# Optimization experiments

Measured on AMD Instinct MI355X. Metric: run time of the kernel, lower is better.

Reference implementation:

```python
import jax, jax.numpy as jnp
import numpy as np

N, E, G, H = 50000, 800000, 2048, 128
DIS = 3  # dis_emb is None -> raw frac_diff (3 dims)
EIN = 2 * H + 6 + DIS  # 265


def _lin_init(key, fan_in, fan_out):
    lim = 1.0 / np.sqrt(fan_in)
    return jax.random.uniform(key, (fan_in, fan_out), jnp.float32, -lim, lim)


def setup_inputs() -> dict:
    key = jax.random.key(0)
    ks = jax.random.split(key, 12)
    node_features = jax.random.normal(ks[0], (N, H), jnp.float32)
    frac_coords = jax.random.uniform(ks[1], (N, 3), jnp.float32)
    lattices = jax.random.normal(ks[2], (G, 6), jnp.float32)
    frac_diff = jax.random.normal(ks[3], (E, 3), jnp.float32)
    edge_index = jax.random.randint(ks[4], (2, E), 0, N, jnp.int64 if jax.config.jax_enable_x64 else jnp.int32)
    edge2graph = jax.random.randint(ks[5], (E,), 0, G, edge_index.dtype)
    return dict(
        node_features=node_features,
        frac_coords=frac_coords,
        lattices=lattices,
        frac_diff=frac_diff,
        edge_index=edge_index,
        edge2graph=edge2graph,
        e_w1=_lin_init(ks[6], EIN, H), e_b1=jnp.zeros((H,), jnp.float32),
        e_w2=_lin_init(ks[7], H, H), e_b2=jnp.zeros((H,), jnp.float32),
        n_w1=_lin_init(ks[8], 2 * H, H), n_b1=jnp.zeros((H,), jnp.float32),
        n_w2=_lin_init(ks[9], H, H), n_b2=jnp.zeros((H,), jnp.float32),
    )


def reference(node_features, frac_coords, lattices, frac_diff, edge_index, edge2graph,
              e_w1, e_b1, e_w2, e_b2, n_w1, n_b1, n_w2, n_b2):
    n_nodes = node_features.shape[0]
    silu = jax.nn.silu
    # edge model: gather endpoints, concat with per-graph lattice + frac_diff
    hi = node_features[edge_index[0]]            # [E, H]
    hj = node_features[edge_index[1]]            # [E, H]
    lat = lattices[edge2graph]                   # [E, 6]
    edges_input = jnp.concatenate([hi, hj, lat, frac_diff], axis=1)  # [E, 265]
    e = silu(edges_input @ e_w1 + e_b1)
    edge_features = silu(e @ e_w2 + e_b2)        # [E, H]
    # scatter-mean aggregate onto source nodes
    seg = edge_index[0]
    agg_sum = jax.ops.segment_sum(edge_features, seg, num_segments=n_nodes)
    cnt = jax.ops.segment_sum(jnp.ones((edge_features.shape[0],), edge_features.dtype), seg, num_segments=n_nodes)
    agg = agg_sum / jnp.maximum(cnt, 1.0)[:, None]
    # node model + residual
    h = jnp.concatenate([node_features, agg], axis=1)  # [N, 2H]
    h = silu(h @ n_w1 + n_b1)
    node_output = silu(h @ n_w2 + n_b2)
    return node_features + node_output
```

## Files before the change

### kernel.cpp

```cpp
#include <hip/hip_runtime.h>

#define N_NODES 50000
#define N_EDGES 800000
#define HDIM 128
#define N_GRAPH 2048

typedef __bf16 bf16x8 __attribute__((ext_vector_type(8)));
typedef float f32x4 __attribute__((ext_vector_type(4)));
typedef float f32x16 __attribute__((ext_vector_type(16)));

static __device__ __forceinline__ unsigned short f2bf(float f) {
    unsigned int u = __float_as_uint(f);
    u += 0x7fffu + ((u >> 16) & 1u);
    return (unsigned short)(u >> 16);
}
static __device__ __forceinline__ float bflo(unsigned int u) { return __uint_as_float(u << 16); }
static __device__ __forceinline__ float bfhi(unsigned int u) { return __uint_as_float(u & 0xFFFF0000u); }

static __device__ __forceinline__ unsigned int cvt_pk_bf16(float lo, float hi) {
    unsigned int r;
    asm("v_cvt_pk_bf16_f32 %0, %1, %2" : "=v"(r) : "v"(lo), "v"(hi));
    return r;
}

static __device__ __forceinline__ float silu_f(float x) {
    float e = __builtin_amdgcn_exp2f(x * -1.44269504f);
    return x * __builtin_amdgcn_rcpf(1.0f + e);
}

#define PREP_BLOCKS 1408
#define HIST_BLOCKS 3125
#define ZERO_BLOCKS 6250
__global__ void prep_hist_kernel(const float* __restrict__ ew1, const float* __restrict__ ew2,
                                 const float* __restrict__ nw1, const float* __restrict__ nw2,
                                 const float* __restrict__ eb1, const float* __restrict__ lattices,
                                 const int* __restrict__ eidx,
                                 unsigned short* __restrict__ W1aT, unsigned short* __restrict__ W1bT,
                                 unsigned short* __restrict__ W2t, unsigned short* __restrict__ N1t,
                                 unsigned short* __restrict__ N2t, unsigned short* __restrict__ Lb,
                                 int* __restrict__ buf, float* __restrict__ agg) {
    const int bid = blockIdx.x;
    if (bid >= PREP_BLOCKS + HIST_BLOCKS) {
        const int idx = (bid - PREP_BLOCKS - HIST_BLOCKS) * 256 + threadIdx.x;
        ((float4*)agg)[idx] = make_float4(0.f, 0.f, 0.f, 0.f);
        return;
    }
    if (bid >= PREP_BLOCKS) {
        int e = (bid - PREP_BLOCKS) * 256 + threadIdx.x;
        if (e < N_EDGES) atomicAdd(&buf[eidx[e]], 1);
        return;
    }
    int i = bid * 256 + threadIdx.x;
    if (i < 16384) {
        int n = i >> 7, k = i & 127;
        W1aT[i] = f2bf(ew1[k * 128 + n]);
    } else if (i < 32768) {
        int j = i - 16384; int n = j >> 7, k = j & 127;
        W1bT[j] = f2bf(ew1[(128 + k) * 128 + n]);
    } else if (i < 49152) {
        int j = i - 32768; int n = j >> 7, k = j & 127;
        W2t[j] = f2bf(ew2[k * 128 + n]);
    } else if (i < 81920) {
        int j = i - 49152; int n = j >> 8, k = j & 255;
        N1t[j] = f2bf(nw1[k * 128 + n]);
    } else if (i < 98304) {
        int j = i - 81920; int n = j >> 7, k = j & 127;
        N2t[j] = f2bf(nw2[k * 128 + n]);
    } else if (i < 98304 + 262144) {
        int j = i - 98304; int g = j >> 7, c = j & 127;
        float s = eb1[c];
#pragma unroll
        for (int t = 0; t < 6; ++t) s += lattices[g * 6 + t] * ew1[(256 + t) * 128 + c];
        Lb[j] = f2bf(s);
    }
}

__global__ __launch_bounds__(1024) void scan_kernel(int* __restrict__ buf) {
    constexpr int CH = 12288;
    __shared__ int lds[CH];
    __shared__ int part[1024];
    __shared__ int carry_s;
    const int t = threadIdx.x;
    if (t == 0) carry_s = 0;
    __syncthreads();
#pragma unroll 1
    for (int base = 0; base < N_NODES; base += CH) {
#pragma unroll
        for (int k = 0; k < CH / 1024; ++k) {
            int f = k * 1024 + t;
            lds[f] = (base + f < N_NODES) ? buf[base + f] : 0;
        }
        __syncthreads();
        int loc[12];
        int s = 0;
#pragma unroll
        for (int i = 0; i < 12; ++i) { loc[i] = lds[t * 12 + i]; s += loc[i]; }
        part[t] = s;
        __syncthreads();
        for (int off = 1; off < 1024; off <<= 1) {
            int tmp = (t >= off) ? part[t - off] : 0;
            __syncthreads();
            part[t] += tmp;
            __syncthreads();
        }
        const int total = part[1023];
        int run = carry_s + part[t] - s;
#pragma unroll
        for (int i = 0; i < 12; ++i) { int tmp = loc[i]; lds[t * 12 + i] = run; run += tmp; }
        __syncthreads();
#pragma unroll
        for (int k = 0; k < CH / 1024; ++k) {
            int f = k * 1024 + t;
            if (base + f < N_NODES) buf[base + f] = lds[f];
        }
        __syncthreads();
        if (t == 0) carry_s += total;
        __syncthreads();
    }
}

#define PERM_BLOCKS2 3125
#define PQ_BLOCKS ((N_NODES + 63) / 64)
__global__ __launch_bounds__(256, 4) void perm_pq_kernel(
    const int* __restrict__ eidx, const int* __restrict__ e2g,
    const float* __restrict__ frac_diff, int* __restrict__ buf,
    unsigned short* __restrict__ perm_lo, unsigned char* __restrict__ perm_hi,
    uint4* __restrict__ rec, const int packed,
    const float* __restrict__ nf, const unsigned short* __restrict__ W1aT,
    const unsigned short* __restrict__ W1bT,
    unsigned short* __restrict__ P, unsigned short* __restrict__ Qm) {
    constexpr int SA = 136;
    __shared__ unsigned short sm[64 * SA];
    const int bid = blockIdx.x;
    const int tid = threadIdx.x;

    if (bid < PERM_BLOCKS2) {
        int e = bid * 256 + tid;
        if (e < N_EDGES) {
            int s = eidx[e];
            int pos = atomicAdd(&buf[s], 1);
            if (packed) {
                int d = eidx[N_EDGES + e];
                int g = e2g[e];
                unsigned int w0 = (unsigned int)s | ((unsigned int)d << 16);
                unsigned int w1 = (unsigned int)g | ((unsigned int)f2bf(frac_diff[3 * e]) << 16);
                unsigned int w2 = (unsigned int)f2bf(frac_diff[3 * e + 1]) |
                                  ((unsigned int)f2bf(frac_diff[3 * e + 2]) << 16);
                rec[pos] = make_uint4(w0, w1, w2, 0u);
            } else {
                perm_lo[pos] = (unsigned short)(e & 0xFFFF);
                perm_hi[pos] = (unsigned char)(e >> 16);
            }
        }
        return;
    }

    const int n0 = (bid - PERM_BLOCKS2) * 64;
    const int mrow = tid >> 2, q = tid & 3;
    {
        const int node = n0 + mrow;
        unsigned short* row = sm + mrow * SA + q * 32;
        if (node < N_NODES) {
            const float4* a4 = (const float4*)(nf + (size_t)node * HDIM) + q * 8;
#pragma unroll
            for (int j = 0; j < 8; ++j) {
                float4 v = a4[j];
                *(ushort4*)(row + 4 * j) = make_ushort4(f2bf(v.x), f2bf(v.y), f2bf(v.z), f2bf(v.w));
            }
        } else {
#pragma unroll
            for (int j = 0; j < 8; ++j) *(ushort4*)(row + 4 * j) = make_ushort4(0, 0, 0, 0);
        }
    }
    __syncthreads();

    const int wave = tid >> 6, lane = tid & 63;
    const int lr = lane & 15, kq = lane >> 4;
    f32x4 acca[8] = {}, accb[8] = {};
    const int arow = (wave * 16 + lr) * SA;
#pragma unroll
    for (int ks = 0; ks < 128; ks += 32) {
        bf16x8 a = *(const bf16x8*)(sm + arow + ks + kq * 8);
#pragma unroll
        for (int nt = 0; nt < 8; ++nt) {
            bf16x8 ba = *(const bf16x8*)(W1aT + (nt * 16 + lr) * 128 + ks + kq * 8);
            acca[nt] = __builtin_amdgcn_mfma_f32_16x16x32_bf16(a, ba, acca[nt], 0, 0, 0);
            bf16x8 bb = *(const bf16x8*)(W1bT + (nt * 16 + lr) * 128 + ks + kq * 8);
            accb[nt] = __builtin_amdgcn_mfma_f32_16x16x32_bf16(a, bb, accb[nt], 0, 0, 0);
        }
    }
    __syncthreads();

    const int node = n0 + mrow;
#pragma unroll
    for (int nt = 0; nt < 8; ++nt) {
        const int col = nt * 16 + lr;
#pragma unroll
        for (int r = 0; r < 4; ++r)
            sm[(wave * 16 + kq * 4 + r) * SA + col] = f2bf(acca[nt][r]);
    }
    __syncthreads();
    if (node < N_NODES) {
        uint4* dst = (uint4*)(P + (size_t)node * HDIM + q * 32);
        const uint4* srcp = (const uint4*)(sm + mrow * SA + q * 32);
#pragma unroll
        for (int j = 0; j < 4; ++j) dst[j] = srcp[j];
    }
    __syncthreads();
#pragma unroll
    for (int nt = 0; nt < 8; ++nt) {
        const int col = nt * 16 + lr;
#pragma unroll
        for (int r = 0; r < 4; ++r)
            sm[(wave * 16 + kq * 4 + r) * SA + col] = f2bf(accb[nt][r]);
    }
    __syncthreads();
    if (node < N_NODES) {
        uint4* dst = (uint4*)(Qm + (size_t)node * HDIM + q * 32);
        const uint4* srcp = (const uint4*)(sm + mrow * SA + q * 32);
#pragma unroll
        for (int j = 0; j < 4; ++j) dst[j] = srcp[j];
    }
}

#define EDGE_NWG (N_EDGES / 128)
template <bool PACKED>
__global__ __launch_bounds__(256, 3) void edge_kernel(
    const unsigned short* __restrict__ P, const unsigned short* __restrict__ Qm,
    const unsigned short* __restrict__ Lb, const float* __restrict__ frac_diff,
    const int* __restrict__ eidx, const int* __restrict__ e2g,
    const unsigned short* __restrict__ perm_lo, const unsigned char* __restrict__ perm_hi,
    const uint4* __restrict__ rec,
    const float* __restrict__ e_w1, const unsigned short* __restrict__ W2t,
    const float* __restrict__ b2, float* __restrict__ agg) {
    const int tid = threadIdx.x;
    const int wv = tid >> 6, lane = tid & 63;
    const int row = lane & 31, hi = lane >> 5;
    const int base = blockIdx.x * 128 + wv * 32;

    int src, dst, g;
    float fd0, fd1, fd2;
    if (PACKED) {
        const uint4 rv = rec[base + row];
        src = rv.x & 0xFFFF;
        dst = rv.x >> 16;
        g = rv.y & 0xFFFF;
        fd0 = bfhi(rv.y);
        fd1 = bflo(rv.z);
        fd2 = bfhi(rv.z);
    } else {
        const int i = base + row;
        const int e = (int)perm_lo[i] | ((int)perm_hi[i] << 16);
        src = eidx[e];
        dst = eidx[N_EDGES + e];
        g = e2g[e];
        fd0 = frac_diff[3 * e];
        fd1 = frac_diff[3 * e + 1];
        fd2 = frac_diff[3 * e + 2];
    }

    const size_t prow = (size_t)src * HDIM;
    const size_t qrow = (size_t)dst * HDIM;
    const size_t lrow = (size_t)g * HDIM;
    uint4 pu[8], qu[8], lu[8];
#pragma unroll
    for (int kk = 0; kk < 8; ++kk) {
        const int c0 = kk * 16 + hi * 8;
        pu[kk] = *(const uint4*)(P + prow + c0);
        qu[kk] = *(const uint4*)(Qm + qrow + c0);
        lu[kk] = *(const uint4*)(Lb + lrow + c0);
    }

    int sc[16], snq[4];
#pragma unroll
    for (int r = 0; r < 16; ++r)
        sc[r] = __shfl(src, (r & 3) + 8 * (r >> 2) + 4 * hi);
#pragma unroll
    for (int j = 0; j < 4; ++j)
        snq[j] = __shfl(src, (4 * (2 * j + hi) + 4) & 31);

    const float* wrbase = e_w1 + 262 * HDIM;
    bf16x8 afrag[8];
#pragma unroll
    for (int kk = 0; kk < 8; ++kk) {
        const int c0 = kk * 16 + hi * 8;
        float w0[8], w1[8], w2[8];
        *(float4*)(w0) = *(const float4*)(wrbase + c0);
        *(float4*)(w0 + 4) = *(const float4*)(wrbase + c0 + 4);
        *(float4*)(w1) = *(const float4*)(wrbase + 128 + c0);
        *(float4*)(w1 + 4) = *(const float4*)(wrbase + 128 + c0 + 4);
        *(float4*)(w2) = *(const float4*)(wrbase + 256 + c0);
        *(float4*)(w2 + 4) = *(const float4*)(wrbase + 256 + c0 + 4);
        const unsigned int* pw = (const unsigned int*)&pu[kk];
        const unsigned int* qw = (const unsigned int*)&qu[kk];
        const unsigned int* lw = (const unsigned int*)&lu[kk];
        unsigned int ow[4];
#pragma unroll
        for (int w = 0; w < 4; ++w) {
            float x0 = bflo(pw[w]) + bflo(qw[w]) + bflo(lw[w])
                     + fd0 * w0[2 * w] + fd1 * w1[2 * w] + fd2 * w2[2 * w];
            float x1 = bfhi(pw[w]) + bfhi(qw[w]) + bfhi(lw[w])
                     + fd0 * w0[2 * w + 1] + fd1 * w1[2 * w + 1] + fd2 * w2[2 * w + 1];
            ow[w] = cvt_pk_bf16(silu_f(x0), silu_f(x1));
        }
        afrag[kk] = *(bf16x8*)ow;
    }

    f32x16 acc[4] = {};
#pragma unroll
    for (int kk = 0; kk < 8; ++kk) {
#pragma unroll
        for (int t4 = 0; t4 < 4; ++t4) {
            bf16x8 bb = *(const bf16x8*)(W2t + (t4 * 32 + row) * 128 + kk * 16 + hi * 8);
            acc[t4] = __builtin_amdgcn_mfma_f32_32x32x16_bf16(afrag[kk], bb, acc[t4], 0, 0, 0);
        }
    }

#pragma unroll
    for (int t4 = 0; t4 < 4; ++t4) {
        const int col = t4 * 32 + row;
        const float bias = b2[col];
        float p[16], tq[4], to[4];
#pragma unroll
        for (int rq = 0; rq < 4; ++rq) {
            float s0 = silu_f(acc[t4][4 * rq + 0] + bias);
            float s1 = silu_f(acc[t4][4 * rq + 1] + bias);
            float s2 = silu_f(acc[t4][4 * rq + 2] + bias);
            float s3 = silu_f(acc[t4][4 * rq + 3] + bias);
            p[4 * rq + 0] = s0;
            p[4 * rq + 1] = s0 + s1;
            p[4 * rq + 2] = p[4 * rq + 1] + s2;
            p[4 * rq + 3] = p[4 * rq + 2] + s3;
            tq[rq] = p[4 * rq + 3];
            to[rq] = __shfl_xor(tq[rq], 32);
        }
        float cum = 0.f;
#pragma unroll
        for (int rq = 0; rq < 4; ++rq) {
            const float off = cum + (hi ? to[rq] : 0.f);
            cum += tq[rq] + to[rq];
#pragma unroll
            for (int i = 0; i < 4; ++i) {
                const int r = 4 * rq + i;
                const float val = p[r] + off;
                const int myrow = 4 * (2 * rq + hi) + i;
                const bool lastg = (myrow == 31);
                const int nxt = (i < 3) ? sc[r + 1] : snq[rq];
                const bool bnd = lastg || (sc[r] != nxt);
                if (bnd) {
                    atomicAdd(&agg[(size_t)sc[r] * HDIM + col], val);
                    if (!lastg) atomicAdd(&agg[(size_t)nxt * HDIM + col], -val);
                }
            }
        }
    }
}

__global__ __launch_bounds__(256, 4) void node_kernel(
    const float* __restrict__ nf, const float* __restrict__ agg,
    const int* __restrict__ buf,
    const unsigned short* __restrict__ N1t, const float* __restrict__ b1,
    const unsigned short* __restrict__ N2t, const float* __restrict__ b2,
    float* __restrict__ out) {
    constexpr int SA = 264;
    constexpr int S2 = 136;
    constexpr int SFo = 132;
    __shared__ unsigned short sm[64 * SA];
    float* smf = (float*)sm;

    const int tid = threadIdx.x;
    const int n0 = blockIdx.x * 64;
    const int mrow = tid >> 2, q = tid & 3;
    {
        const int node = n0 + mrow;
        unsigned short* row = sm + mrow * SA;
        const int cbq = q * 32;
        if (node < N_NODES) {
            const int c = buf[node] - (node ? buf[node - 1] : 0);
            const float inv = 1.0f / (float)max(c, 1);
            const float4* a4 = (const float4*)(nf + (size_t)node * HDIM) + q * 8;
            const float4* g4 = (const float4*)(agg + (size_t)node * HDIM) + q * 8;
#pragma unroll
            for (int j = 0; j < 8; ++j) {
                float4 v = a4[j];
                *(ushort4*)(row + cbq + 4 * j) =
                    make_ushort4(f2bf(v.x), f2bf(v.y), f2bf(v.z), f2bf(v.w));
                float4 g = g4[j];
                *(ushort4*)(row + HDIM + cbq + 4 * j) =
                    make_ushort4(f2bf(g.x * inv), f2bf(g.y * inv), f2bf(g.z * inv), f2bf(g.w * inv));
            }
        } else {
#pragma unroll
            for (int j = 0; j < 8; ++j) {
                *(ushort4*)(row + cbq + 4 * j) = make_ushort4(0, 0, 0, 0);
                *(ushort4*)(row + HDIM + cbq + 4 * j) = make_ushort4(0, 0, 0, 0);
            }
        }
    }
    __syncthreads();

    const int wave = tid >> 6, lane = tid & 63;
    const int lr = lane & 15, kq = lane >> 4;

    f32x4 acc[8] = {};
    const int arow = (wave * 16 + lr) * SA;
#pragma unroll
    for (int ks = 0; ks < 256; ks += 32) {
        bf16x8 a = *(const bf16x8*)(sm + arow + ks + kq * 8);
#pragma unroll
        for (int nt = 0; nt < 8; ++nt) {
            bf16x8 bb = *(const bf16x8*)(N1t + (nt * 16 + lr) * 256 + ks + kq * 8);
            acc[nt] = __builtin_amdgcn_mfma_f32_16x16x32_bf16(a, bb, acc[nt], 0, 0, 0);
        }
    }
    __syncthreads();

#pragma unroll
    for (int nt = 0; nt < 8; ++nt) {
        const int col = nt * 16 + lr;
        const float bias = b1[col];
#pragma unroll
        for (int r = 0; r < 4; ++r) {
            const int mm = wave * 16 + kq * 4 + r;
            sm[mm * S2 + col] = f2bf(silu_f(acc[nt][r] + bias));
        }
    }
    __syncthreads();

    f32x4 acc2[8] = {};
    const int arow2 = (wave * 16 + lr) * S2;
#pragma unroll
    for (int ks = 0; ks < 128; ks += 32) {
        bf16x8 a = *(const bf16x8*)(sm + arow2 + ks + kq * 8);
#pragma unroll
        for (int nt = 0; nt < 8; ++nt) {
            bf16x8 bb = *(const bf16x8*)(N2t + (nt * 16 + lr) * 128 + ks + kq * 8);
            acc2[nt] = __builtin_amdgcn_mfma_f32_16x16x32_bf16(a, bb, acc2[nt], 0, 0, 0);
        }
    }
    __syncthreads();

#pragma unroll
    for (int nt = 0; nt < 8; ++nt) {
        const int col = nt * 16 + lr;
        const float bias = b2[col];
#pragma unroll
        for (int r = 0; r < 4; ++r) {
            const int mm = wave * 16 + kq * 4 + r;
            smf[mm * SFo + col] = silu_f(acc2[nt][r] + bias);
        }
    }
    __syncthreads();
    {
        const int node = n0 + mrow;
        if (node < N_NODES) {
            const float4* nfr = (const float4*)(nf + (size_t)node * HDIM) + q * 8;
            float4* outr = (float4*)(out + (size_t)node * HDIM) + q * 8;
            const float* st = smf + mrow * SFo + q * 32;
#pragma unroll
            for (int j = 0; j < 8; ++j) {
                float4 v = nfr[j];
                float4 s4 = *(const float4*)(st + 4 * j);
                v.x += s4.x; v.y += s4.y; v.z += s4.z; v.w += s4.w;
                outr[j] = v;
            }
        }
    }
}

extern "C" void kernel_launch(void* const* d_in, const int* in_sizes, int n_in,
                              void* d_out, int out_size, void* d_ws, size_t ws_size,
                              hipStream_t stream) {
    const float* node_features = (const float*)d_in[0];
    const float* lattices = (const float*)d_in[2];
    const float* frac_diff = (const float*)d_in[3];
    const int* edge_index = (const int*)d_in[4];
    const int* edge2graph = (const int*)d_in[5];
    const float* e_w1 = (const float*)d_in[6];
    const float* e_b1 = (const float*)d_in[7];
    const float* e_w2 = (const float*)d_in[8];
    const float* e_b2 = (const float*)d_in[9];
    const float* n_w1 = (const float*)d_in[10];
    const float* n_b1 = (const float*)d_in[11];
    const float* n_w2 = (const float*)d_in[12];
    const float* n_b2 = (const float*)d_in[13];

    char* ws = (char*)d_ws;
    unsigned short* W1aT = (unsigned short*)(ws);
    unsigned short* W1bT = (unsigned short*)(ws + 32768);
    unsigned short* W2t  = (unsigned short*)(ws + 65536);
    unsigned short* N1t  = (unsigned short*)(ws + 98304);
    unsigned short* N2t  = (unsigned short*)(ws + 163840);
    unsigned short* Lb   = (unsigned short*)(ws + 196608);
    unsigned short* P    = (unsigned short*)(ws + 720896);
    unsigned short* Qm   = (unsigned short*)(ws + 13520896);
    int* buf             = (int*)(ws + 26320896);
    unsigned short* perm_lo = (unsigned short*)(ws + 26520896);
    unsigned char* perm_hi  = (unsigned char*)(ws + 28120896);
    uint4* rec           = (uint4*)(ws + 28920896);
    float* agg = (float*)d_out;

    const int packed = (ws_size >= 28920896 + (size_t)N_EDGES * 16) ? 1 : 0;

    hipMemsetAsync(buf, 0, (size_t)N_NODES * 4, stream);

    prep_hist_kernel<<<PREP_BLOCKS + HIST_BLOCKS + ZERO_BLOCKS, 256, 0, stream>>>(
        e_w1, e_w2, n_w1, n_w2, e_b1, lattices, edge_index,
        W1aT, W1bT, W2t, N1t, N2t, Lb, buf, agg);

    scan_kernel<<<1, 1024, 0, stream>>>(buf);

    perm_pq_kernel<<<PERM_BLOCKS2 + PQ_BLOCKS, 256, 0, stream>>>(
        edge_index, edge2graph, frac_diff, buf, perm_lo, perm_hi, rec, packed,
        node_features, W1aT, W1bT, P, Qm);

    if (packed) {
        edge_kernel<true><<<EDGE_NWG, 256, 0, stream>>>(
            P, Qm, Lb, frac_diff, edge_index, edge2graph, perm_lo, perm_hi, rec,
            e_w1, W2t, e_b2, agg);
    } else {
        edge_kernel<false><<<EDGE_NWG, 256, 0, stream>>>(
            P, Qm, Lb, frac_diff, edge_index, edge2graph, perm_lo, perm_hi, rec,
            e_w1, W2t, e_b2, agg);
    }

    node_kernel<<<(N_NODES + 63) / 64, 256, 0, stream>>>(
        node_features, agg, buf, N1t, n_b1, N2t, n_b2, (float*)d_out);
}
```

Baseline: 544.4 us.

## Process two 32-edge tiles per wave with prefetched gathers and LDS-staged frac weights

Each wave in the edge kernel now handles two 32-edge tiles and issues the gathers for both tiles up front, so the second tile's global loads overlap with the first tile's compute. The frac_diff rows of the first-layer weights are converted to bf16 once per block and read from LDS, replacing per-lane fp32 global loads. The price is more registers per wave (occupancy bound drops from 3 to 2), one block-wide barrier, and slightly lower precision on those weights.

Result: faster. 515.1 us (-5.4%).

```diff
diff --git a/kernel.cpp b/kernel.cpp
--- a/kernel.cpp
+++ b/kernel.cpp
@@ -223,90 +223,39 @@
     }
 }
 
-#define EDGE_NWG (N_EDGES / 128)
-template <bool PACKED>
-__global__ __launch_bounds__(256, 3) void edge_kernel(
-    const unsigned short* __restrict__ P, const unsigned short* __restrict__ Qm,
-    const unsigned short* __restrict__ Lb, const float* __restrict__ frac_diff,
-    const int* __restrict__ eidx, const int* __restrict__ e2g,
-    const unsigned short* __restrict__ perm_lo, const unsigned char* __restrict__ perm_hi,
-    const uint4* __restrict__ rec,
-    const float* __restrict__ e_w1, const unsigned short* __restrict__ W2t,
-    const float* __restrict__ b2, float* __restrict__ agg) {
-    const int tid = threadIdx.x;
-    const int wv = tid >> 6, lane = tid & 63;
-    const int row = lane & 31, hi = lane >> 5;
-    const int base = blockIdx.x * 128 + wv * 32;
-
-    int src, dst, g;
-    float fd0, fd1, fd2;
-    if (PACKED) {
-        const uint4 rv = rec[base + row];
-        src = rv.x & 0xFFFF;
-        dst = rv.x >> 16;
-        g = rv.y & 0xFFFF;
-        fd0 = bfhi(rv.y);
-        fd1 = bflo(rv.z);
-        fd2 = bfhi(rv.z);
-    } else {
-        const int i = base + row;
-        const int e = (int)perm_lo[i] | ((int)perm_hi[i] << 16);
-        src = eidx[e];
-        dst = eidx[N_EDGES + e];
-        g = e2g[e];
-        fd0 = frac_diff[3 * e];
-        fd1 = frac_diff[3 * e + 1];
-        fd2 = frac_diff[3 * e + 2];
-    }
-
-    const size_t prow = (size_t)src * HDIM;
-    const size_t qrow = (size_t)dst * HDIM;
-    const size_t lrow = (size_t)g * HDIM;
-    uint4 pu[8], qu[8], lu[8];
+
+static __device__ __forceinline__ void build_afrag(
+    const uint4* pu, const uint4* qu, const uint4* lu,
+    float f0, float f1, float f2,
+    const unsigned int* wlds, int hi, bf16x8* afrag) {
 #pragma unroll
     for (int kk = 0; kk < 8; ++kk) {
-        const int c0 = kk * 16 + hi * 8;
-        pu[kk] = *(const uint4*)(P + prow + c0);
-        qu[kk] = *(const uint4*)(Qm + qrow + c0);
-        lu[kk] = *(const uint4*)(Lb + lrow + c0);
-    }
-
-    int sc[16], snq[4];
-#pragma unroll
-    for (int r = 0; r < 16; ++r)
-        sc[r] = __shfl(src, (r & 3) + 8 * (r >> 2) + 4 * hi);
-#pragma unroll
-    for (int j = 0; j < 4; ++j)
-        snq[j] = __shfl(src, (4 * (2 * j + hi) + 4) & 31);
-
-    const float* wrbase = e_w1 + 262 * HDIM;
-    bf16x8 afrag[8];
-#pragma unroll
-    for (int kk = 0; kk < 8; ++kk) {
-        const int c0 = kk * 16 + hi * 8;
-        float w0[8], w1[8], w2[8];
-        *(float4*)(w0) = *(const float4*)(wrbase + c0);
-        *(float4*)(w0 + 4) = *(const float4*)(wrbase + c0 + 4);
-        *(float4*)(w1) = *(const float4*)(wrbase + 128 + c0);
-        *(float4*)(w1 + 4) = *(const float4*)(wrbase + 128 + c0 + 4);
-        *(float4*)(w2) = *(const float4*)(wrbase + 256 + c0);
-        *(float4*)(w2 + 4) = *(const float4*)(wrbase + 256 + c0 + 4);
+        const unsigned int* wl = wlds + (kk * 2 + hi) * 12;
+        const uint4 w0v = *(const uint4*)(wl);
+        const uint4 w1v = *(const uint4*)(wl + 4);
+        const uint4 w2v = *(const uint4*)(wl + 8);
         const unsigned int* pw = (const unsigned int*)&pu[kk];
         const unsigned int* qw = (const unsigned int*)&qu[kk];
         const unsigned int* lw = (const unsigned int*)&lu[kk];
+        const unsigned int* w0w = (const unsigned int*)&w0v;
+        const unsigned int* w1w = (const unsigned int*)&w1v;
+        const unsigned int* w2w = (const unsigned int*)&w2v;
         unsigned int ow[4];
 #pragma unroll
         for (int w = 0; w < 4; ++w) {
             float x0 = bflo(pw[w]) + bflo(qw[w]) + bflo(lw[w])
-                     + fd0 * w0[2 * w] + fd1 * w1[2 * w] + fd2 * w2[2 * w];
+                     + f0 * bflo(w0w[w]) + f1 * bflo(w1w[w]) + f2 * bflo(w2w[w]);
             float x1 = bfhi(pw[w]) + bfhi(qw[w]) + bfhi(lw[w])
-                     + fd0 * w0[2 * w + 1] + fd1 * w1[2 * w + 1] + fd2 * w2[2 * w + 1];
+                     + f0 * bfhi(w0w[w]) + f1 * bfhi(w1w[w]) + f2 * bfhi(w2w[w]);
             ow[w] = cvt_pk_bf16(silu_f(x0), silu_f(x1));
         }
         afrag[kk] = *(bf16x8*)ow;
     }
-
-    f32x16 acc[4] = {};
+}
+
+static __device__ __forceinline__ void do_mfma(
+    const bf16x8* afrag, const unsigned short* __restrict__ W2t,
+    int row, int hi, f32x16* acc) {
 #pragma unroll
     for (int kk = 0; kk < 8; ++kk) {
 #pragma unroll
@@ -315,7 +264,11 @@
             acc[t4] = __builtin_amdgcn_mfma_f32_32x32x16_bf16(afrag[kk], bb, acc[t4], 0, 0, 0);
         }
     }
-
+}
+
+static __device__ __forceinline__ void epilogue(
+    const f32x16* acc, const int* sc, const int* snq,
+    int row, int hi, const float* __restrict__ b2, float* __restrict__ agg) {
 #pragma unroll
     for (int t4 = 0; t4 < 4; ++t4) {
         const int col = t4 * 32 + row;
@@ -354,6 +307,112 @@
             }
         }
     }
+}
+
+#define EDGE_NWG (N_EDGES / 256)
+template <bool PACKED>
+static __device__ __forceinline__ void fetch_meta(
+    int i, const uint4* __restrict__ rec, const int* __restrict__ eidx,
+    const int* __restrict__ e2g, const float* __restrict__ frac_diff,
+    const unsigned short* __restrict__ perm_lo, const unsigned char* __restrict__ perm_hi,
+    int& src, int& dst, int& g, float& f0, float& f1, float& f2) {
+    if (PACKED) {
+        const uint4 rv = rec[i];
+        src = rv.x & 0xFFFF;
+        dst = rv.x >> 16;
+        g = rv.y & 0xFFFF;
+        f0 = bfhi(rv.y);
+        f1 = bflo(rv.z);
+        f2 = bfhi(rv.z);
+    } else {
+        const int e = (int)perm_lo[i] | ((int)perm_hi[i] << 16);
+        src = eidx[e];
+        dst = eidx[N_EDGES + e];
+        g = e2g[e];
+        f0 = frac_diff[3 * e];
+        f1 = frac_diff[3 * e + 1];
+        f2 = frac_diff[3 * e + 2];
+    }
+}
+
+template <bool PACKED>
+__global__ __launch_bounds__(256, 2) void edge_kernel(
+    const unsigned short* __restrict__ P, const unsigned short* __restrict__ Qm,
+    const unsigned short* __restrict__ Lb, const float* __restrict__ frac_diff,
+    const int* __restrict__ eidx, const int* __restrict__ e2g,
+    const unsigned short* __restrict__ perm_lo, const unsigned char* __restrict__ perm_hi,
+    const uint4* __restrict__ rec,
+    const float* __restrict__ e_w1, const unsigned short* __restrict__ W2t,
+    const float* __restrict__ b2, float* __restrict__ agg) {
+    __shared__ __align__(16) unsigned int wlds[192];
+    const int tid = threadIdx.x;
+    {
+        const float* wrbase = e_w1 + 262 * HDIM;
+        if (tid < 192) {
+            const int w = tid & 3, rw = (tid >> 2) % 3, hi = (tid / 12) & 1, kk = tid / 24;
+            const int c = kk * 16 + hi * 8 + 2 * w;
+            wlds[((kk * 2 + hi) * 3 + rw) * 4 + w] =
+                (unsigned int)f2bf(wrbase[rw * HDIM + c]) |
+                ((unsigned int)f2bf(wrbase[rw * HDIM + c + 1]) << 16);
+        }
+    }
+    __syncthreads();
+
+    const int wv = tid >> 6, lane = tid & 63;
+    const int row = lane & 31, hi = lane >> 5;
+    const int base = blockIdx.x * 256 + wv * 64;
+
+    int srcA, dstA, gA; float fA0, fA1, fA2;
+    fetch_meta<PACKED>(base + row, rec, eidx, e2g, frac_diff, perm_lo, perm_hi,
+                       srcA, dstA, gA, fA0, fA1, fA2);
+    int srcB, dstB, gB; float fB0, fB1, fB2;
+    fetch_meta<PACKED>(base + 32 + row, rec, eidx, e2g, frac_diff, perm_lo, perm_hi,
+                       srcB, dstB, gB, fB0, fB1, fB2);
+
+    uint4 puA[8], quA[8], luA[8];
+    {
+        const size_t pr = (size_t)srcA * HDIM, qr = (size_t)dstA * HDIM, lr = (size_t)gA * HDIM;
+#pragma unroll
+        for (int kk = 0; kk < 8; ++kk) {
+            const int c0 = kk * 16 + hi * 8;
+            puA[kk] = *(const uint4*)(P + pr + c0);
+            quA[kk] = *(const uint4*)(Qm + qr + c0);
+            luA[kk] = *(const uint4*)(Lb + lr + c0);
+        }
+    }
+    uint4 puB[8], quB[8], luB[8];
+    {
+        const size_t pr = (size_t)srcB * HDIM, qr = (size_t)dstB * HDIM, lr = (size_t)gB * HDIM;
+#pragma unroll
+        for (int kk = 0; kk < 8; ++kk) {
+            const int c0 = kk * 16 + hi * 8;
+            puB[kk] = *(const uint4*)(P + pr + c0);
+            quB[kk] = *(const uint4*)(Qm + qr + c0);
+            luB[kk] = *(const uint4*)(Lb + lr + c0);
+        }
+    }
+
+    bf16x8 afragA[8];
+    build_afrag(puA, quA, luA, fA0, fA1, fA2, wlds, hi, afragA);
+    int scA[16], snqA[4];
+#pragma unroll
+    for (int r = 0; r < 16; ++r) scA[r] = __shfl(srcA, (r & 3) + 8 * (r >> 2) + 4 * hi);
+#pragma unroll
+    for (int j = 0; j < 4; ++j) snqA[j] = __shfl(srcA, (4 * (2 * j + hi) + 4) & 31);
+    f32x16 accA[4] = {};
+    do_mfma(afragA, W2t, row, hi, accA);
+    epilogue(accA, scA, snqA, row, hi, b2, agg);
+
+    bf16x8 afragB[8];
+    build_afrag(puB, quB, luB, fB0, fB1, fB2, wlds, hi, afragB);
+    int scB[16], snqB[4];
+#pragma unroll
+    for (int r = 0; r < 16; ++r) scB[r] = __shfl(srcB, (r & 3) + 8 * (r >> 2) + 4 * hi);
+#pragma unroll
+    for (int j = 0; j < 4; ++j) snqB[j] = __shfl(srcB, (4 * (2 * j + hi) + 4) & 31);
+    f32x16 accB[4] = {};
+    do_mfma(afragB, W2t, row, hi, accB);
+    epilogue(accB, scB, snqB, row, hi, b2, agg);
 }
 
 __global__ __launch_bounds__(256, 4) void node_kernel(
```
